# Kernel optimization log

Measured on AMD Instinct MI355X. Metric: run time of the kernel, lower is better.

The kernel has to match this reference:

```python
import jax, jax.numpy as jnp
import numpy as np

E, CAP, D, H = 8, 2048, 1024, 4096  # experts, capacity, model_dim, hidden

def setup_inputs() -> dict:
    key = jax.random.key(0)
    k = jax.random.split(key, 5)
    s1 = 1.0 / np.sqrt(D)
    s2 = 1.0 / np.sqrt(H)
    return {
        "x": jax.random.normal(k[0], (E, CAP, D), dtype=jnp.float32),
        "fc1_w": jax.random.uniform(k[1], (E, H, D), jnp.float32, -s1, s1),
        "fc1_b": jax.random.uniform(k[2], (E, H), jnp.float32, -s1, s1),
        "fc2_w": jax.random.uniform(k[3], (E, H, D), jnp.float32, -s2, s2),
        "fc2_b": jax.random.uniform(k[4], (E, D), jnp.float32, -s2, s2),
    }

def reference(x, fc1_w, fc1_b, fc2_w, fc2_b):
    # y = relu(x @ fc1_w^T + b1) @ fc2_w + b2, batched over experts e
    y = jnp.einsum('ecd,ehd->ech', x, fc1_w) + fc1_b[:, None, :]   # [E, CAP, H]
    y = jax.nn.relu(y)
    y = jnp.einsum('ech,ehd->ecd', y, fc2_w) + fc2_b[:, None, :]   # [E, CAP, D]
    return y
```

## Files before the change

kernel.cpp:

```cpp
#include <hip/hip_runtime.h>
#include <hip/hip_bf16.h>
#include <stdint.h>

#define E_    8
#define CAP_  2048
#define D_    1024
#define H_    4096

typedef unsigned short u16;
typedef __attribute__((ext_vector_type(8))) short bf16x8;
typedef __attribute__((ext_vector_type(4))) float f32x4;

__device__ __forceinline__ u16 f2bf(float f) {
    union { float f; unsigned int u; } v; v.f = f;
    unsigned int u = v.u;
    unsigned int r = (u + 0x7fffu + ((u >> 16) & 1u)) >> 16;
    return (u16)r;
}

__device__ __forceinline__ void gload_lds16(const void* g, void* l) {
    __builtin_amdgcn_global_load_lds(
        (const __attribute__((address_space(1))) unsigned int*)g,
        (__attribute__((address_space(3))) unsigned int*)l,
        16, 0, 0);
}

__global__ void cvt_f32_bf16(const float* __restrict__ in, u16* __restrict__ out, int n4) {
    int i = blockIdx.x * blockDim.x + threadIdx.x;
    if (i >= n4) return;
    const float4 v = ((const float4*)in)[i];
    ushort4 o;
    o.x = f2bf(v.x); o.y = f2bf(v.y); o.z = f2bf(v.z); o.w = f2bf(v.w);
    ((ushort4*)out)[i] = o;
}

__global__ void transpose_cvt(const float* __restrict__ in, u16* __restrict__ out) {
    __shared__ float t[64][69];
    const int e  = blockIdx.z;
    const int h0 = blockIdx.y * 64;
    const int d0 = blockIdx.x * 64;
    const float* I = in + (size_t)e * H_ * D_;
    u16* O = out + (size_t)e * D_ * H_;
    const int tid = threadIdx.x;
    const int r  = tid >> 4;
    const int c  = (tid & 15) * 4;
    #pragma unroll
    for (int s = 0; s < 4; ++s) {
        const int h = r + s * 16;
        const float4 v = *(const float4*)&I[(size_t)(h0 + h) * D_ + d0 + c];
        t[h][c] = v.x; t[h][c + 1] = v.y; t[h][c + 2] = v.z; t[h][c + 3] = v.w;
    }
    __syncthreads();
    #pragma unroll
    for (int s = 0; s < 4; ++s) {
        const int d = r + s * 16;
        ushort4 o;
        o.x = f2bf(t[c + 0][d]); o.y = f2bf(t[c + 1][d]);
        o.z = f2bf(t[c + 2][d]); o.w = f2bf(t[c + 3][d]);
        *(ushort4*)&O[(size_t)(d0 + d) * H_ + h0 + c] = o;
    }
}

template<int EPI>
__global__ __launch_bounds__(512, 2) void gemm256(
    const u16* __restrict__ A, const u16* __restrict__ B,
    const float* __restrict__ bias, void* __restrict__ Cv,
    int M, int N, int K, int TM, int TN,
    size_t sA, size_t sB, size_t sBias, size_t sC)
{
    __shared__ __align__(16) u16 lds[2][2][2][128 * 64];

    const int nwg = gridDim.x;
    const int cpx = nwg >> 3;
    const int bid = blockIdx.x;
    const int wg  = (bid & 7) * cpx + (bid >> 3);
    const int tpe = TM * TN;
    const int e   = wg / tpe;
    const int rem = wg - e * tpe;
    const int tn  = rem / TM;
    const int tm  = rem - tn * TM;
    const int row0 = tm << 8;
    const int col0 = tn << 8;

    const u16* Ae = A + (size_t)e * sA;
    const u16* Be = B + (size_t)e * sB;

    const int tid  = threadIdx.x;
    const int lane = tid & 63;
    const int w    = tid >> 6;
    const int wr   = w >> 2;
    const int wc   = w & 3;
    const int wcH  = wc >> 1;
    const int wcL  = wc & 1;
    const int fr   = lane & 15;
    const int fq   = lane >> 4;
    const int cx   = (fq ^ (fr & 7)) << 4;
    const int lo0  = fr * 128 + cx;
    const int lo1  = fr * 128 + (cx ^ 64);
    const int sl   = lane ^ ((lane >> 3) & 7);
    const int NT   = K >> 6;

    const int srow = (w << 4) + (sl >> 3);
    const int scol = (sl & 7) << 3;
    const u16* pA[2][2];
    const u16* pB[2][2];
    #pragma unroll
    for (int l = 0; l < 2; ++l)
        #pragma unroll
        for (int hf = 0; hf < 2; ++hf) {
            pA[l][hf] = Ae + (size_t)(row0 + hf * 128 + srow + l * 8) * K + scol;
            pB[l][hf] = Be + (size_t)(col0 + hf * 128 + srow + l * 8) * K + scol;
        }

    auto stage = [&](int buf, bool pred) {
        #pragma unroll
        for (int l = 0; l < 2; ++l)
            #pragma unroll
            for (int hf = 0; hf < 2; ++hf) {
                if (pred) {
                    gload_lds16(pA[l][hf], &lds[buf][0][hf][(w * 2 + l) * 512]);
                    gload_lds16(pB[l][hf], &lds[buf][1][hf][(w * 2 + l) * 512]);
                }
                pA[l][hf] += 64;
                pB[l][hf] += 64;
            }
    };

    f32x4 acc[8][4] = {};

    stage(0, true);
    asm volatile("s_waitcnt vmcnt(0)");
    __builtin_amdgcn_s_barrier();

    for (int t = 0; t < NT; ++t) {
        const int db = t & 1;
        const char* Ah = (const char*)&lds[db][0][wr][0];
        const char* Bh = (const char*)&lds[db][1][wcH][0];

        auto rdA = [&](bf16x8 (&a)[2][2], int p) {
            #pragma unroll
            for (int mm = 0; mm < 2; ++mm) {
                a[mm][0] = *(const bf16x8*)(Ah + (2 * p + mm) * 2048 + lo0);
                a[mm][1] = *(const bf16x8*)(Ah + (2 * p + mm) * 2048 + lo1);
            }
        };

        bf16x8 b[4][2];
        #pragma unroll
        for (int n = 0; n < 4; ++n) {
            b[n][0] = *(const bf16x8*)(Bh + wcL * 8192 + n * 2048 + lo0);
            b[n][1] = *(const bf16x8*)(Bh + wcL * 8192 + n * 2048 + lo1);
        }

        auto domfma = [&](bf16x8 (&a)[2][2], int p) {
            __builtin_amdgcn_s_setprio(1);
            #pragma unroll
            for (int kk = 0; kk < 2; ++kk)
                #pragma unroll
                for (int mm = 0; mm < 2; ++mm)
                    #pragma unroll
                    for (int n = 0; n < 4; ++n)
                        acc[2 * p + mm][n] = __builtin_amdgcn_mfma_f32_16x16x32_bf16(
                            a[mm][kk], b[n][kk], acc[2 * p + mm][n], 0, 0, 0);
            __builtin_amdgcn_s_setprio(0);
        };

        bf16x8 aA[2][2], aB[2][2];
        rdA(aA, 0);
        stage(db ^ 1, t + 1 < NT);
        rdA(aB, 1); domfma(aA, 0);
        rdA(aA, 2); domfma(aB, 1);
        rdA(aB, 3); domfma(aA, 2);
        domfma(aB, 3);

        asm volatile("s_waitcnt vmcnt(0)");
        __builtin_amdgcn_s_barrier();
    }

    const float* be = bias + (size_t)e * sBias;
    if (EPI == 0) {
        u16* cl = (u16*)&lds[0][0][0][0];
        #pragma unroll
        for (int n = 0; n < 4; ++n) {
            const int ccol = wc * 64 + n * 16 + fr;
            const float bv = be[col0 + ccol];
            #pragma unroll
            for (int m = 0; m < 8; ++m) {
                const int crow = wr * 128 + m * 16 + fq * 4;
                #pragma unroll
                for (int i = 0; i < 4; ++i) {
                    float v = acc[m][n][i] + bv;
                    v = v > 0.f ? v : 0.f;
                    cl[(crow + i) * 256 + ccol] = f2bf(v);
                }
            }
        }
        __builtin_amdgcn_s_barrier();
        u16* Ce = (u16*)Cv + (size_t)e * sC;
        const int rr = tid >> 5;
        const int cc = (tid & 31) * 8;
        #pragma unroll
        for (int s = 0; s < 16; ++s) {
            const int row = s * 16 + rr;
            const float4 v = *(const float4*)&cl[row * 256 + cc];
            *(float4*)&Ce[(size_t)(row0 + row) * N + col0 + cc] = v;
        }
    } else {
        float* cf = (float*)&lds[0][0][0][0];
        float* Ce = (float*)Cv + (size_t)e * sC;
        #pragma unroll
        for (int p = 0; p < 2; ++p) {
            __builtin_amdgcn_s_barrier();
            #pragma unroll
            for (int n = 0; n < 4; ++n) {
                const int ccol = wc * 64 + n * 16 + fr;
                const float bv = be[col0 + ccol];
                #pragma unroll
                for (int mm = 0; mm < 4; ++mm) {
                    const int lrow = wr * 64 + mm * 16 + fq * 4;
                    #pragma unroll
                    for (int i = 0; i < 4; ++i)
                        cf[(lrow + i) * 256 + ccol] = acc[p * 4 + mm][n][i] + bv;
                }
            }
            __builtin_amdgcn_s_barrier();
            const int lr = tid >> 6;
            const int cc = (tid & 63) * 4;
            #pragma unroll
            for (int s = 0; s < 16; ++s) {
                const int lrow = s * 8 + lr;
                const int wrr  = lrow >> 6;
                const int rem2 = lrow & 63;
                const int grow = row0 + wrr * 128 + p * 64 + rem2;
                const float4 v = *(const float4*)&cf[lrow * 256 + cc];
                *(float4*)&Ce[(size_t)grow * N + col0 + cc] = v;
            }
        }
    }
}

extern "C" void kernel_launch(void* const* d_in, const int* in_sizes, int n_in,
                              void* d_out, int out_size, void* d_ws, size_t ws_size,
                              hipStream_t stream) {
    (void)in_sizes; (void)n_in; (void)out_size; (void)ws_size;
    const float* x     = (const float*)d_in[0];
    const float* fc1_w = (const float*)d_in[1];
    const float* fc1_b = (const float*)d_in[2];
    const float* fc2_w = (const float*)d_in[3];
    const float* fc2_b = (const float*)d_in[4];
    float* out = (float*)d_out;

    u16* xbf  = (u16*)d_ws;
    u16* w1bf = xbf  + (size_t)E_ * CAP_ * D_;
    u16* w2t  = w1bf + (size_t)E_ * H_ * D_;
    u16* y1   = w2t  + (size_t)E_ * D_ * H_;

    {
        int n4 = E_ * CAP_ * D_ / 4;
        cvt_f32_bf16<<<n4 / 256, 256, 0, stream>>>(x, xbf, n4);
    }
    {
        int n4 = E_ * H_ * D_ / 4;
        cvt_f32_bf16<<<n4 / 256, 256, 0, stream>>>(fc1_w, w1bf, n4);
    }
    transpose_cvt<<<dim3(D_ / 64, H_ / 64, E_), 256, 0, stream>>>(fc2_w, w2t);

    gemm256<0><<<dim3(E_ * (CAP_ / 256) * (H_ / 256)), 512, 0, stream>>>(
        xbf, w1bf, fc1_b, y1, CAP_, H_, D_, CAP_ / 256, H_ / 256,
        (size_t)CAP_ * D_, (size_t)H_ * D_, (size_t)H_, (size_t)CAP_ * H_);

    gemm256<1><<<dim3(E_ * (CAP_ / 256) * (D_ / 256)), 512, 0, stream>>>(
        y1, w2t, fc2_b, out, CAP_, D_, H_, CAP_ / 256, D_ / 256,
        (size_t)CAP_ * H_, (size_t)D_ * H_, (size_t)D_, (size_t)CAP_ * D_);
}
```

Before: 366.4 us.

## Load full A/B fragments per tile and interleave with MFMA via sched_group_barrier

Each K-tile now reads all A and B fragments from LDS into registers up front instead of in alternating half-buffers. Explicit sched_group_barrier directives interleave the LDS reads, global-to-LDS loads and MFMAs. The staging predicate is replaced by clamping the next-tile offset, so the last iteration reloads the final tile rather than branching. The aim is better hiding of LDS and global latency behind MFMA issue, at the cost of higher register pressure and a redundant load on the last iteration.

```diff
diff --git a/kernel.cpp b/kernel.cpp
--- a/kernel.cpp
+++ b/kernel.cpp
@@ -112,23 +112,19 @@
             pB[l][hf] = Be + (size_t)(col0 + hf * 128 + srow + l * 8) * K + scol;
         }
 
-    auto stage = [&](int buf, bool pred) {
+    auto stage = [&](int buf, int koff) {
         #pragma unroll
         for (int l = 0; l < 2; ++l)
             #pragma unroll
             for (int hf = 0; hf < 2; ++hf) {
-                if (pred) {
-                    gload_lds16(pA[l][hf], &lds[buf][0][hf][(w * 2 + l) * 512]);
-                    gload_lds16(pB[l][hf], &lds[buf][1][hf][(w * 2 + l) * 512]);
-                }
-                pA[l][hf] += 64;
-                pB[l][hf] += 64;
+                gload_lds16(pA[l][hf] + koff, &lds[buf][0][hf][(w * 2 + l) * 512]);
+                gload_lds16(pB[l][hf] + koff, &lds[buf][1][hf][(w * 2 + l) * 512]);
             }
     };
 
     f32x4 acc[8][4] = {};
 
-    stage(0, true);
+    stage(0, 0);
     asm volatile("s_waitcnt vmcnt(0)");
     __builtin_amdgcn_s_barrier();
 
@@ -136,24 +132,39 @@
         const int db = t & 1;
         const char* Ah = (const char*)&lds[db][0][wr][0];
         const char* Bh = (const char*)&lds[db][1][wcH][0];
-
-        auto rdA = [&](bf16x8 (&a)[2][2], int p) {
-            #pragma unroll
-            for (int mm = 0; mm < 2; ++mm) {
-                a[mm][0] = *(const bf16x8*)(Ah + (2 * p + mm) * 2048 + lo0);
-                a[mm][1] = *(const bf16x8*)(Ah + (2 * p + mm) * 2048 + lo1);
-            }
-        };
-
-        bf16x8 b[4][2];
-        #pragma unroll
-        for (int n = 0; n < 4; ++n) {
-            b[n][0] = *(const bf16x8*)(Bh + wcL * 8192 + n * 2048 + lo0);
-            b[n][1] = *(const bf16x8*)(Bh + wcL * 8192 + n * 2048 + lo1);
-        }
-
-        auto domfma = [&](bf16x8 (&a)[2][2], int p) {
-            __builtin_amdgcn_s_setprio(1);
+        const char* Bq = Bh + wcL * 8192;
+
+        bf16x8 a[8][2], b[4][2];
+        b[0][0] = *(const bf16x8*)(Bq + 0 * 2048 + lo0);
+        b[1][0] = *(const bf16x8*)(Bq + 1 * 2048 + lo0);
+        b[2][0] = *(const bf16x8*)(Bq + 2 * 2048 + lo0);
+        b[3][0] = *(const bf16x8*)(Bq + 3 * 2048 + lo0);
+        a[0][0] = *(const bf16x8*)(Ah + 0 * 2048 + lo0);
+        a[1][0] = *(const bf16x8*)(Ah + 1 * 2048 + lo0);
+        b[0][1] = *(const bf16x8*)(Bq + 0 * 2048 + lo1);
+        b[1][1] = *(const bf16x8*)(Bq + 1 * 2048 + lo1);
+        b[2][1] = *(const bf16x8*)(Bq + 2 * 2048 + lo1);
+        b[3][1] = *(const bf16x8*)(Bq + 3 * 2048 + lo1);
+        a[0][1] = *(const bf16x8*)(Ah + 0 * 2048 + lo1);
+        a[1][1] = *(const bf16x8*)(Ah + 1 * 2048 + lo1);
+        a[2][0] = *(const bf16x8*)(Ah + 2 * 2048 + lo0);
+        a[3][0] = *(const bf16x8*)(Ah + 3 * 2048 + lo0);
+        a[2][1] = *(const bf16x8*)(Ah + 2 * 2048 + lo1);
+        a[3][1] = *(const bf16x8*)(Ah + 3 * 2048 + lo1);
+        a[4][0] = *(const bf16x8*)(Ah + 4 * 2048 + lo0);
+        a[5][0] = *(const bf16x8*)(Ah + 5 * 2048 + lo0);
+        a[4][1] = *(const bf16x8*)(Ah + 4 * 2048 + lo1);
+        a[5][1] = *(const bf16x8*)(Ah + 5 * 2048 + lo1);
+        a[6][0] = *(const bf16x8*)(Ah + 6 * 2048 + lo0);
+        a[7][0] = *(const bf16x8*)(Ah + 7 * 2048 + lo0);
+        a[6][1] = *(const bf16x8*)(Ah + 6 * 2048 + lo1);
+        a[7][1] = *(const bf16x8*)(Ah + 7 * 2048 + lo1);
+
+        const int nx = (t + 1 < NT - 1) ? (t + 1) : (NT - 1);
+        stage(db ^ 1, nx * 64);
+
+        #pragma unroll
+        for (int p = 0; p < 4; ++p)
             #pragma unroll
             for (int kk = 0; kk < 2; ++kk)
                 #pragma unroll
@@ -161,17 +172,18 @@
                     #pragma unroll
                     for (int n = 0; n < 4; ++n)
                         acc[2 * p + mm][n] = __builtin_amdgcn_mfma_f32_16x16x32_bf16(
-                            a[mm][kk], b[n][kk], acc[2 * p + mm][n], 0, 0, 0);
-            __builtin_amdgcn_s_setprio(0);
-        };
-
-        bf16x8 aA[2][2], aB[2][2];
-        rdA(aA, 0);
-        stage(db ^ 1, t + 1 < NT);
-        rdA(aB, 1); domfma(aA, 0);
-        rdA(aA, 2); domfma(aB, 1);
-        rdA(aB, 3); domfma(aA, 2);
-        domfma(aB, 3);
+                            a[2 * p + mm][kk], b[n][kk], acc[2 * p + mm][n], 0, 0, 0);
+
+        __builtin_amdgcn_sched_group_barrier(0x100, 6, 0);
+        __builtin_amdgcn_sched_group_barrier(0x008, 8, 0);
+        __builtin_amdgcn_sched_group_barrier(0x100, 6, 0);
+        __builtin_amdgcn_sched_group_barrier(0x008, 8, 0);
+        #pragma unroll
+        for (int i = 0; i < 12; ++i) {
+            __builtin_amdgcn_sched_group_barrier(0x100, 1, 0);
+            if (i < 8) __builtin_amdgcn_sched_group_barrier(0x010, 1, 0);
+            __builtin_amdgcn_sched_group_barrier(0x008, 4, 0);
+        }
 
         asm volatile("s_waitcnt vmcnt(0)");
         __builtin_amdgcn_s_barrier();
```

After: 414.8 us. +13.2%, slower.

## Prefetch next tile's LDS fragments before final MFMA group in software pipeline

Applied to the files above, without the earlier changes.

Restructures the GEMM main loop into a two-iteration unrolled body with ping-pong B register sets. After the third MFMA group it waits on the global->LDS copy and a barrier, then reads the next tile's B and first A fragments while the last MFMA group runs. A second barrier protects the buffer being reused. The goal is to hide LDS read latency at the start of each K-step, at the cost of more registers and an extra barrier per iteration. It assumes NT is even.

```diff
diff --git a/kernel.cpp b/kernel.cpp
--- a/kernel.cpp
+++ b/kernel.cpp
@@ -127,54 +127,63 @@
     };
 
     f32x4 acc[8][4] = {};
+    bf16x8 bX[4][2], bY[4][2], aC[2][2], aX[2][2];
+
+    auto rdA = [&](bf16x8 (&dst)[2][2], const char* Ah, int p) {
+        dst[0][0] = *(const bf16x8*)(Ah + (2 * p + 0) * 2048 + lo0);
+        dst[0][1] = *(const bf16x8*)(Ah + (2 * p + 0) * 2048 + lo1);
+        dst[1][0] = *(const bf16x8*)(Ah + (2 * p + 1) * 2048 + lo0);
+        dst[1][1] = *(const bf16x8*)(Ah + (2 * p + 1) * 2048 + lo1);
+    };
+    auto rdB = [&](bf16x8 (&dst)[4][2], const char* Bq) {
+        #pragma unroll
+        for (int n = 0; n < 4; ++n) {
+            dst[n][0] = *(const bf16x8*)(Bq + n * 2048 + lo0);
+            dst[n][1] = *(const bf16x8*)(Bq + n * 2048 + lo1);
+        }
+    };
+    auto mf = [&](bf16x8 (&a)[2][2], bf16x8 (&b)[4][2], int p) {
+        __builtin_amdgcn_s_setprio(1);
+        #pragma unroll
+        for (int kk = 0; kk < 2; ++kk)
+            #pragma unroll
+            for (int mm = 0; mm < 2; ++mm)
+                #pragma unroll
+                for (int n = 0; n < 4; ++n)
+                    acc[2 * p + mm][n] = __builtin_amdgcn_mfma_f32_16x16x32_bf16(
+                        a[mm][kk], b[n][kk], acc[2 * p + mm][n], 0, 0, 0);
+        __builtin_amdgcn_s_setprio(0);
+    };
+
+    auto body = [&](int db, bf16x8 (&bCur)[4][2], bf16x8 (&bNxt)[4][2], int t) {
+        const char* Ah  = (const char*)&lds[db][0][wr][0];
+        const char* Bq  = (const char*)&lds[db][1][wcH][0] + wcL * 8192;
+        const char* AhN = (const char*)&lds[db ^ 1][0][wr][0];
+        const char* BqN = (const char*)&lds[db ^ 1][1][wcH][0] + wcL * 8192;
+
+        stage(db ^ 1, t + 1 < NT);
+
+        rdA(aX, Ah, 1); mf(aC, bCur, 0);
+        rdA(aC, Ah, 2); mf(aX, bCur, 1);
+        rdA(aX, Ah, 3); mf(aC, bCur, 2);
+        asm volatile("s_waitcnt vmcnt(0)");
+        __builtin_amdgcn_s_barrier();
+        __builtin_amdgcn_sched_barrier(0);
+        rdB(bNxt, BqN);
+        rdA(aC, AhN, 0);
+        mf(aX, bCur, 3);
+        __builtin_amdgcn_s_barrier();
+    };
 
     stage(0, true);
     asm volatile("s_waitcnt vmcnt(0)");
     __builtin_amdgcn_s_barrier();
-
-    for (int t = 0; t < NT; ++t) {
-        const int db = t & 1;
-        const char* Ah = (const char*)&lds[db][0][wr][0];
-        const char* Bh = (const char*)&lds[db][1][wcH][0];
-
-        auto rdA = [&](bf16x8 (&a)[2][2], int p) {
-            #pragma unroll
-            for (int mm = 0; mm < 2; ++mm) {
-                a[mm][0] = *(const bf16x8*)(Ah + (2 * p + mm) * 2048 + lo0);
-                a[mm][1] = *(const bf16x8*)(Ah + (2 * p + mm) * 2048 + lo1);
-            }
-        };
-
-        bf16x8 b[4][2];
-        #pragma unroll
-        for (int n = 0; n < 4; ++n) {
-            b[n][0] = *(const bf16x8*)(Bh + wcL * 8192 + n * 2048 + lo0);
-            b[n][1] = *(const bf16x8*)(Bh + wcL * 8192 + n * 2048 + lo1);
-        }
-
-        auto domfma = [&](bf16x8 (&a)[2][2], int p) {
-            __builtin_amdgcn_s_setprio(1);
-            #pragma unroll
-            for (int kk = 0; kk < 2; ++kk)
-                #pragma unroll
-                for (int mm = 0; mm < 2; ++mm)
-                    #pragma unroll
-                    for (int n = 0; n < 4; ++n)
-                        acc[2 * p + mm][n] = __builtin_amdgcn_mfma_f32_16x16x32_bf16(
-                            a[mm][kk], b[n][kk], acc[2 * p + mm][n], 0, 0, 0);
-            __builtin_amdgcn_s_setprio(0);
-        };
-
-        bf16x8 aA[2][2], aB[2][2];
-        rdA(aA, 0);
-        stage(db ^ 1, t + 1 < NT);
-        rdA(aB, 1); domfma(aA, 0);
-        rdA(aA, 2); domfma(aB, 1);
-        rdA(aB, 3); domfma(aA, 2);
-        domfma(aB, 3);
-
-        asm volatile("s_waitcnt vmcnt(0)");
-        __builtin_amdgcn_s_barrier();
+    rdB(bX, (const char*)&lds[0][1][wcH][0] + wcL * 8192);
+    rdA(aC, (const char*)&lds[0][0][wr][0], 0);
+
+    for (int t = 0; t < NT; t += 2) {
+        body(0, bX, bY, t);
+        body(1, bY, bX, t + 1);
     }
 
     const float* be = bias + (size_t)e * sBias;
```

Result: slower. 537.0 us (+46.6%).

## Switch GEMM inner loop from 16x16x32 to 32x32x16 bf16 MFMA tiles

Applied to the files above, without the earlier changes.

Replaces the 16x16x32 MFMA tiling (8x4 accumulators of 4 floats) with 32x32x16 MFMA (4x2 accumulators of 16 floats). LDS read offsets, the swizzle and the epilogue row/column mapping are reworked to match. The larger MFMA tile needs fewer LDS fragment reads per flop and fewer MFMA issues. The software-pipelined interleave of A reads with MFMAs is simplified to a plain per-row-tile loop, which may expose more LDS latency.

```diff
diff --git a/kernel.cpp b/kernel.cpp
--- a/kernel.cpp
+++ b/kernel.cpp
@@ -9,7 +9,7 @@
 
 typedef unsigned short u16;
 typedef __attribute__((ext_vector_type(8))) short bf16x8;
-typedef __attribute__((ext_vector_type(4))) float f32x4;
+typedef __attribute__((ext_vector_type(16))) float f32x16;
 
 __device__ __forceinline__ u16 f2bf(float f) {
     union { float f; unsigned int u; } v; v.f = f;
@@ -92,11 +92,13 @@
     const int wc   = w & 3;
     const int wcH  = wc >> 1;
     const int wcL  = wc & 1;
-    const int fr   = lane & 15;
-    const int fq   = lane >> 4;
-    const int cx   = (fq ^ (fr & 7)) << 4;
-    const int lo0  = fr * 128 + cx;
-    const int lo1  = fr * 128 + (cx ^ 64);
+    const int rr   = lane & 31;
+    const int hi   = lane >> 5;
+    const int sw   = rr & 7;
+    const int L0   = rr * 128 + (((0 | hi) ^ sw) << 4);
+    const int L1   = rr * 128 + (((2 | hi) ^ sw) << 4);
+    const int L2   = rr * 128 + (((4 | hi) ^ sw) << 4);
+    const int L3   = rr * 128 + (((6 | hi) ^ sw) << 4);
     const int sl   = lane ^ ((lane >> 3) & 7);
     const int NT   = K >> 6;
 
@@ -126,7 +128,7 @@
             }
     };
 
-    f32x4 acc[8][4] = {};
+    f32x16 acc[4][2] = {};
 
     stage(0, true);
     asm volatile("s_waitcnt vmcnt(0)");
@@ -135,43 +137,35 @@
     for (int t = 0; t < NT; ++t) {
         const int db = t & 1;
         const char* Ah = (const char*)&lds[db][0][wr][0];
-        const char* Bh = (const char*)&lds[db][1][wcH][0];
-
-        auto rdA = [&](bf16x8 (&a)[2][2], int p) {
-            #pragma unroll
-            for (int mm = 0; mm < 2; ++mm) {
-                a[mm][0] = *(const bf16x8*)(Ah + (2 * p + mm) * 2048 + lo0);
-                a[mm][1] = *(const bf16x8*)(Ah + (2 * p + mm) * 2048 + lo1);
-            }
-        };
-
-        bf16x8 b[4][2];
-        #pragma unroll
-        for (int n = 0; n < 4; ++n) {
-            b[n][0] = *(const bf16x8*)(Bh + wcL * 8192 + n * 2048 + lo0);
-            b[n][1] = *(const bf16x8*)(Bh + wcL * 8192 + n * 2048 + lo1);
-        }
-
-        auto domfma = [&](bf16x8 (&a)[2][2], int p) {
+        const char* Bq = (const char*)&lds[db][1][wcH][0] + wcL * 8192;
+
+        stage(db ^ 1, t + 1 < NT);
+
+        bf16x8 b[2][4];
+        #pragma unroll
+        for (int nt = 0; nt < 2; ++nt) {
+            b[nt][0] = *(const bf16x8*)(Bq + nt * 4096 + L0);
+            b[nt][1] = *(const bf16x8*)(Bq + nt * 4096 + L1);
+            b[nt][2] = *(const bf16x8*)(Bq + nt * 4096 + L2);
+            b[nt][3] = *(const bf16x8*)(Bq + nt * 4096 + L3);
+        }
+
+        #pragma unroll
+        for (int mt = 0; mt < 4; ++mt) {
+            bf16x8 a[4];
+            a[0] = *(const bf16x8*)(Ah + mt * 4096 + L0);
+            a[1] = *(const bf16x8*)(Ah + mt * 4096 + L1);
+            a[2] = *(const bf16x8*)(Ah + mt * 4096 + L2);
+            a[3] = *(const bf16x8*)(Ah + mt * 4096 + L3);
             __builtin_amdgcn_s_setprio(1);
             #pragma unroll
-            for (int kk = 0; kk < 2; ++kk)
+            for (int ks = 0; ks < 4; ++ks)
                 #pragma unroll
-                for (int mm = 0; mm < 2; ++mm)
-                    #pragma unroll
-                    for (int n = 0; n < 4; ++n)
-                        acc[2 * p + mm][n] = __builtin_amdgcn_mfma_f32_16x16x32_bf16(
-                            a[mm][kk], b[n][kk], acc[2 * p + mm][n], 0, 0, 0);
+                for (int nt = 0; nt < 2; ++nt)
+                    acc[mt][nt] = __builtin_amdgcn_mfma_f32_32x32x16_bf16(
+                        a[ks], b[nt][ks], acc[mt][nt], 0, 0, 0);
             __builtin_amdgcn_s_setprio(0);
-        };
-
-        bf16x8 aA[2][2], aB[2][2];
-        rdA(aA, 0);
-        stage(db ^ 1, t + 1 < NT);
-        rdA(aB, 1); domfma(aA, 0);
-        rdA(aA, 2); domfma(aB, 1);
-        rdA(aB, 3); domfma(aA, 2);
-        domfma(aB, 3);
+        }
 
         asm volatile("s_waitcnt vmcnt(0)");
         __builtin_amdgcn_s_barrier();
@@ -181,27 +175,27 @@
     if (EPI == 0) {
         u16* cl = (u16*)&lds[0][0][0][0];
         #pragma unroll
-        for (int n = 0; n < 4; ++n) {
-            const int ccol = wc * 64 + n * 16 + fr;
+        for (int nt = 0; nt < 2; ++nt) {
+            const int ccol = wc * 64 + nt * 32 + rr;
             const float bv = be[col0 + ccol];
             #pragma unroll
-            for (int m = 0; m < 8; ++m) {
-                const int crow = wr * 128 + m * 16 + fq * 4;
+            for (int mt = 0; mt < 4; ++mt) {
                 #pragma unroll
-                for (int i = 0; i < 4; ++i) {
-                    float v = acc[m][n][i] + bv;
+                for (int reg = 0; reg < 16; ++reg) {
+                    const int crow = wr * 128 + mt * 32 + (reg & 3) + 8 * (reg >> 2) + 4 * hi;
+                    float v = acc[mt][nt][reg] + bv;
                     v = v > 0.f ? v : 0.f;
-                    cl[(crow + i) * 256 + ccol] = f2bf(v);
+                    cl[crow * 256 + ccol] = f2bf(v);
                 }
             }
         }
         __builtin_amdgcn_s_barrier();
         u16* Ce = (u16*)Cv + (size_t)e * sC;
-        const int rr = tid >> 5;
+        const int rw = tid >> 5;
         const int cc = (tid & 31) * 8;
         #pragma unroll
         for (int s = 0; s < 16; ++s) {
-            const int row = s * 16 + rr;
+            const int row = s * 16 + rw;
             const float4 v = *(const float4*)&cl[row * 256 + cc];
             *(float4*)&Ce[(size_t)(row0 + row) * N + col0 + cc] = v;
         }
@@ -212,15 +206,17 @@
         for (int p = 0; p < 2; ++p) {
             __builtin_amdgcn_s_barrier();
             #pragma unroll
-            for (int n = 0; n < 4; ++n) {
-                const int ccol = wc * 64 + n * 16 + fr;
+            for (int nt = 0; nt < 2; ++nt) {
+                const int ccol = wc * 64 + nt * 32 + rr;
                 const float bv = be[col0 + ccol];
                 #pragma unroll
-                for (int mm = 0; mm < 4; ++mm) {
-                    const int lrow = wr * 64 + mm * 16 + fq * 4;
+                for (int mh = 0; mh < 2; ++mh) {
+                    const int mt = 2 * p + mh;
                     #pragma unroll
-                    for (int i = 0; i < 4; ++i)
-                        cf[(lrow + i) * 256 + ccol] = acc[p * 4 + mm][n][i] + bv;
+                    for (int reg = 0; reg < 16; ++reg) {
+                        const int lrow = wr * 64 + mh * 32 + (reg & 3) + 8 * (reg >> 2) + 4 * hi;
+                        cf[lrow * 256 + ccol] = acc[mt][nt][reg] + bv;
+                    }
                 }
             }
             __builtin_amdgcn_s_barrier();
```

After: 374.6 us. 1.02x slower.
